# Kernel optimization log

Measured on AMD Instinct MI355X. Metric: run time of the kernel, lower is better.

The kernel has to match this reference:

```python
import jax, jax.numpy as jnp
import numpy as np
from jax import lax

B, C, H, W = 4, 256, 64, 64
R = 4  # reduction
BN_EPS = 1e-5


def setup_inputs() -> dict:
    key = jax.random.key(0)
    ks = jax.random.split(key, 18)
    n = jax.random.normal
    return {
        "x_self": n(ks[0], (B, C, H, W), jnp.float32),
        "x_other": n(ks[1], (B, C, H, W), jnp.float32),
        "q_w": n(ks[2], (C, C), jnp.float32) * 0.05,      # self_q 1x1 conv
        "q_b": n(ks[3], (C,), jnp.float32) * 0.05,
        "kv_w": n(ks[4], (2 * C, C), jnp.float32) * 0.05,  # other_kv 1x1 conv
        "kv_b": n(ks[5], (2 * C,), jnp.float32) * 0.05,
        "g1_w": n(ks[6], (C // R, C), jnp.float32) * 0.05,  # gate conv1
        "g1_b": n(ks[7], (C // R,), jnp.float32) * 0.05,
        "g2_w": n(ks[8], (1, C // R), jnp.float32) * 0.05,  # gate conv2
        "g2_b": n(ks[9], (1,), jnp.float32) * 0.05,
        "dw_w": n(ks[10], (C, 1, 3, 3), jnp.float32) * 0.1,  # depthwise 3x3
        "dw_b": n(ks[11], (C,), jnp.float32) * 0.05,
        "bn_g": jnp.ones((C,), jnp.float32),
        "bn_b": jnp.zeros((C,), jnp.float32),
        "bn_m": n(ks[12], (C,), jnp.float32) * 0.05,
        "bn_v": jax.random.uniform(ks[13], (C,), jnp.float32, 0.5, 1.5),
        "out_w": n(ks[14], (C, C), jnp.float32) * 0.05,
        "out_b": n(ks[15], (C,), jnp.float32) * 0.05,
    }


def _conv1x1(x, w, b):
    return jnp.einsum('bchw,oc->bohw', x, w) + b[None, :, None, None]


def reference(x_self, x_other, q_w, q_b, kv_w, kv_b, g1_w, g1_b, g2_w, g2_b,
              dw_w, dw_b, bn_g, bn_b, bn_m, bn_v, out_w, out_b):
    # local branch: depthwise 3x3 conv -> BatchNorm (eval stats) -> SiLU
    y = lax.conv_general_dilated(
        x_self, dw_w, (1, 1), 'SAME',
        feature_group_count=C,
        dimension_numbers=('NCHW', 'OIHW', 'NCHW')) + dw_b[None, :, None, None]
    scale = (bn_g / jnp.sqrt(bn_v + BN_EPS))[None, :, None, None]
    y = (y - bn_m[None, :, None, None]) * scale + bn_b[None, :, None, None]
    local_feat = y * jax.nn.sigmoid(y)  # SiLU

    # cross attention over HW tokens
    q = _conv1x1(x_self, q_w, q_b).reshape(B, C, H * W)
    kv = _conv1x1(x_other, kv_w, kv_b)
    k = kv[:, :C].reshape(B, C, H * W)
    v = kv[:, C:].reshape(B, C, H * W)
    attn = jnp.einsum('bcn,bcm->bnm', q, k) / jnp.sqrt(jnp.float32(C))  # [B,HW,HW]
    attn = jax.nn.softmax(attn, axis=-1)
    attn_out = jnp.einsum('bnm,bcm->bcn', attn, v).reshape(B, C, H, W)

    # channel-squeeze gate on x_self -> scalar per sample
    p = jnp.mean(x_self, axis=(2, 3))                 # [B,C] global avg pool
    g = jax.nn.relu(p @ g1_w.T + g1_b)                # [B,C//R]
    g = jax.nn.sigmoid(g @ g2_w.T + g2_b)             # [B,1]
    gate = g[:, :, None, None]

    fused = local_feat + gate * attn_out
    return _conv1x1(fused, out_w, out_b)
```

## Files before the change

### kernel.cpp

```cpp
#include <hip/hip_runtime.h>
#include <stdint.h>

#define BB 4
#define CC 256
#define HH 64
#define WWD 64
#define NN 4096
#define LOG2E 1.4426950408889634f

typedef __attribute__((ext_vector_type(8))) short short8;
typedef __attribute__((ext_vector_type(4))) float f32x4;
typedef __attribute__((ext_vector_type(16))) float f32x16;
typedef __attribute__((ext_vector_type(4))) unsigned short us4;
typedef unsigned long long ull;

__device__ __forceinline__ unsigned short f2bf(float f) {
  unsigned int u = __float_as_uint(f);
  u += 0x7fffu + ((u >> 16) & 1u);
  return (unsigned short)(u >> 16);
}
__device__ __forceinline__ float bf2f(unsigned short h) {
  return __uint_as_float(((unsigned int)h) << 16);
}
__device__ __forceinline__ short8 ld8(const unsigned short* p) {
  return *reinterpret_cast<const short8*>(p);
}
__device__ __forceinline__ unsigned char f2fp8(float v) {
  return (unsigned char)__builtin_amdgcn_cvt_pk_fp8_f32(v, v, 0, false);
}
__device__ __forceinline__ int rowmap(int reg, int h) {
  return (reg & 3) + 8 * (reg >> 2) + 4 * h;
}

__global__ __launch_bounds__(256, 2) void k_pre(
    const float* __restrict__ xs, const float* __restrict__ xo,
    const float* __restrict__ dww, const float* __restrict__ dwb,
    const float* __restrict__ bng, const float* __restrict__ bnb,
    const float* __restrict__ bnm, const float* __restrict__ bnv,
    const float* __restrict__ qw, const float* __restrict__ kvw,
    const float* __restrict__ ow, unsigned short* __restrict__ XtS,
    unsigned short* __restrict__ XtO, unsigned short* __restrict__ localT,
    float* __restrict__ psumA, unsigned short* __restrict__ Wb) {
  __shared__ float rb3[3][64][67];
  __shared__ unsigned short sb[64][67];
  int tid = threadIdx.x;
  if (blockIdx.z == 8) {
    int i = (blockIdx.x * 64 + blockIdx.y) * 1024 + tid * 4;
    const float* src;
    if (i < 65536) src = qw + i;
    else if (i < 196608) src = kvw + (i - 65536);
    else src = ow + (i - 196608);
    f32x4 v = *reinterpret_cast<const f32x4*>(src);
    us4 r;
#pragma unroll
    for (int j = 0; j < 4; ++j) r[j] = f2bf(v[j]);
    *reinterpret_cast<us4*>(Wb + i) = r;
    return;
  }
  int c0 = blockIdx.x * 64, h = blockIdx.y;
  int b = blockIdx.z >> 1, which = blockIdx.z & 1;
  const float* src = which ? xo : xs;
  int wq = tid >> 6, w = tid & 63;
  int dlo = which ? 1 : 0, dhi = which ? 1 : 2;
  for (int d = dlo; d <= dhi; ++d) {
    int hh = h + d - 1;
    bool ok = (hh >= 0 && hh < HH);
#pragma unroll
    for (int p = 0; p < 4; ++p) {
      int idx = p * 256 + tid;
      int cl = idx >> 4, ws4 = (idx & 15) * 4;
      f32x4 v = {};
      if (ok)
        v = *reinterpret_cast<const f32x4*>(
            &src[(((size_t)(b * CC + c0 + cl)) * HH + hh) * WWD + ws4]);
#pragma unroll
      for (int j = 0; j < 4; ++j) rb3[d][cl][ws4 + 1 + j] = v[j];
    }
    if (tid < 64) { rb3[d][tid][0] = 0.f; rb3[d][tid][65] = 0.f; }
  }
  __syncthreads();
  unsigned short* dst = which ? XtO : XtS;
  int n0 = h * 64, cb = (tid & 15) * 4;
#pragma unroll
  for (int i = 0; i < 4; ++i) {
    int wl = i * 16 + (tid >> 4);
    us4 r;
#pragma unroll
    for (int j = 0; j < 4; ++j) r[j] = f2bf(rb3[1][cb + j][wl + 1]);
    *reinterpret_cast<us4*>(&dst[((size_t)b * NN + n0 + wl) * CC + c0 + cb]) = r;
  }
  if (which) return;
  if (tid < 64) {
    float s = 0.f;
    for (int ww = 0; ww < 64; ++ww) s += rb3[1][tid][ww + 1];
    psumA[((size_t)(b * 64 + h)) * CC + c0 + tid] = s;
  }
  for (int p = 0; p < 16; ++p) {
    int cl = p * 4 + wq, c = c0 + cl;
    float acc = 0.f;
#pragma unroll
    for (int di = 0; di < 3; ++di)
#pragma unroll
      for (int dj = 0; dj < 3; ++dj)
        acc = fmaf(rb3[di][cl][w + dj], dww[c * 9 + di * 3 + dj], acc);
    float y = acc + dwb[c];
    float sc = bng[c] * rsqrtf(bnv[c] + 1e-5f);
    float v = (y - bnm[c]) * sc + bnb[c];
    sb[cl][w] = f2bf(v / (1.f + __expf(-v)));
  }
  __syncthreads();
#pragma unroll
  for (int i = 0; i < 4; ++i) {
    int wl = i * 16 + (tid >> 4);
    us4 r;
#pragma unroll
    for (int j = 0; j < 4; ++j) r[j] = sb[cb + j][wl];
    *reinterpret_cast<us4*>(&localT[((size_t)b * NN + h * WWD + wl) * CC + c0 + cb]) = r;
  }
}

__global__ __launch_bounds__(256, 4) void k_qkv(
    const unsigned short* __restrict__ XtS, const unsigned short* __restrict__ XtO,
    const unsigned short* __restrict__ Wb, const float* __restrict__ qb,
    const float* __restrict__ kvb, const float* __restrict__ psumA,
    const float* __restrict__ g1w, const float* __restrict__ g1b,
    const float* __restrict__ g2w, const float* __restrict__ g2b,
    unsigned char* __restrict__ Qt8, unsigned char* __restrict__ Kt8,
    unsigned char* __restrict__ Vv8, float* __restrict__ gate) {
  __shared__ unsigned short Xs[64][264];
  int tid = threadIdx.x;
  int id = blockIdx.y;
  if (id == 3) {
    if (blockIdx.x != 0 || blockIdx.z != 0) return;
    float* mf = (float*)&Xs[0][0];
    float* hpf = mf + 1024;
    int c = tid;
    for (int b4 = 0; b4 < 4; ++b4) {
      float s = 0.f;
      for (int hh = 0; hh < 64; ++hh) s += psumA[((size_t)(b4 * 64 + hh)) * CC + c];
      mf[b4 * 256 + c] = s * (1.f / 4096.f);
    }
    __syncthreads();
    for (int b4 = 0; b4 < 4; ++b4) {
      int j = tid >> 2, cq = tid & 3;
      float s = 0.f;
      for (int cc = cq * 64; cc < cq * 64 + 64; ++cc)
        s = fmaf(mf[b4 * 256 + cc], g1w[j * CC + cc], s);
      hpf[j * 5 + cq] = s;
      __syncthreads();
      if (tid < 64) {
        float hh = fmaxf(hpf[tid * 5] + hpf[tid * 5 + 1] + hpf[tid * 5 + 2] +
                             hpf[tid * 5 + 3] + g1b[tid], 0.f);
        float t = hh * g2w[tid];
        for (int off = 32; off; off >>= 1) t += __shfl_down(t, off, 64);
        if (tid == 0) gate[b4] = 1.f / (1.f + expf(-(t + g2b[0])));
      }
      __syncthreads();
    }
    return;
  }
  int n0 = blockIdx.x * 64, b = blockIdx.z;
  const unsigned short* Xt = (id == 0) ? XtS : XtO;
  const unsigned short* W = Wb + id * 65536;
  int wave = tid >> 6, lane = tid & 63, l31 = lane & 31, h = lane >> 5;
#pragma unroll
  for (int p = 0; p < 8; ++p) {
    int r = p * 8 + (tid >> 5), c = (tid & 31) * 8;
    *reinterpret_cast<uint4*>(&Xs[r][c]) =
        *reinterpret_cast<const uint4*>(Xt + ((size_t)b * NN + n0 + r) * CC + c);
  }
  __syncthreads();
  int o0 = wave * 64;
  f32x16 acc[4] = {};
  if (id < 2) {
#pragma unroll
    for (int t = 0; t < 16; ++t) {
      short8 a0 = ld8(&Xs[l31][t * 16 + h * 8]);
      short8 a1 = ld8(&Xs[32 + l31][t * 16 + h * 8]);
      short8 b0 = ld8(W + (size_t)(o0 + l31) * CC + t * 16 + h * 8);
      short8 b1 = ld8(W + (size_t)(o0 + 32 + l31) * CC + t * 16 + h * 8);
      acc[0] = __builtin_amdgcn_mfma_f32_32x32x16_bf16(a0, b0, acc[0], 0, 0, 0);
      acc[1] = __builtin_amdgcn_mfma_f32_32x32x16_bf16(a0, b1, acc[1], 0, 0, 0);
      acc[2] = __builtin_amdgcn_mfma_f32_32x32x16_bf16(a1, b0, acc[2], 0, 0, 0);
      acc[3] = __builtin_amdgcn_mfma_f32_32x32x16_bf16(a1, b1, acc[3], 0, 0, 0);
    }
    const float* bias = id ? kvb : qb;
    unsigned char* Out8 = id ? Kt8 : Qt8;
    __syncthreads();
    unsigned char (*T8)[264] = reinterpret_cast<unsigned char(*)[264]>(&Xs[0][0]);
#pragma unroll
    for (int nt = 0; nt < 2; ++nt)
#pragma unroll
      for (int ot = 0; ot < 2; ++ot) {
        int o = o0 + ot * 32 + l31;
        float bv = bias[o];
#pragma unroll
        for (int reg = 0; reg < 16; ++reg) {
          int nl = nt * 32 + rowmap(reg, h);
          T8[nl][o] = f2fp8((acc[nt * 2 + ot][reg] + bv) * 0.25f);
        }
      }
    __syncthreads();
#pragma unroll
    for (int p = 0; p < 4; ++p) {
      int idx = p * 256 + tid, row = idx >> 4, cc = (idx & 15) * 16;
      ull a0 = *reinterpret_cast<const ull*>(&T8[row][cc]);
      ull a1 = *reinterpret_cast<const ull*>(&T8[row][cc + 8]);
      uint4 u;
      u.x = (unsigned)a0; u.y = (unsigned)(a0 >> 32);
      u.z = (unsigned)a1; u.w = (unsigned)(a1 >> 32);
      *reinterpret_cast<uint4*>(Out8 + ((size_t)b * NN + n0 + row) * CC + cc) = u;
    }
  } else {
#pragma unroll
    for (int t = 0; t < 16; ++t) {
      short8 a0 = ld8(W + (size_t)(o0 + l31) * CC + t * 16 + h * 8);
      short8 a1 = ld8(W + (size_t)(o0 + 32 + l31) * CC + t * 16 + h * 8);
      short8 b0 = ld8(&Xs[l31][t * 16 + h * 8]);
      short8 b1 = ld8(&Xs[32 + l31][t * 16 + h * 8]);
      acc[0] = __builtin_amdgcn_mfma_f32_32x32x16_bf16(a0, b0, acc[0], 0, 0, 0);
      acc[1] = __builtin_amdgcn_mfma_f32_32x32x16_bf16(a0, b1, acc[1], 0, 0, 0);
      acc[2] = __builtin_amdgcn_mfma_f32_32x32x16_bf16(a1, b0, acc[2], 0, 0, 0);
      acc[3] = __builtin_amdgcn_mfma_f32_32x32x16_bf16(a1, b1, acc[3], 0, 0, 0);
    }
    __syncthreads();
    unsigned char (*V8)[72] = reinterpret_cast<unsigned char(*)[72]>(&Xs[0][0]);
#pragma unroll
    for (int ot = 0; ot < 2; ++ot)
#pragma unroll
      for (int nt = 0; nt < 2; ++nt)
#pragma unroll
        for (int reg = 0; reg < 16; ++reg) {
          int o = o0 + ot * 32 + rowmap(reg, h);
          int nl = nt * 32 + l31;
          V8[o][nl] = f2fp8(acc[ot * 2 + nt][reg] + kvb[CC + o]);
        }
    __syncthreads();
#pragma unroll
    for (int p = 0; p < 4; ++p) {
      int idx = p * 256 + tid, o = idx >> 2, mm = (idx & 3) * 16;
      ull a0 = *reinterpret_cast<const ull*>(&V8[o][mm]);
      ull a1 = *reinterpret_cast<const ull*>(&V8[o][mm + 8]);
      uint4 u;
      u.x = (unsigned)a0; u.y = (unsigned)(a0 >> 32);
      u.z = (unsigned)a1; u.w = (unsigned)(a1 >> 32);
      *reinterpret_cast<uint4*>(Vv8 + ((size_t)b * CC + o) * NN + n0 + mm) = u;
    }
  }
}

__global__ __launch_bounds__(256, 3) void k_flash8(
    const unsigned char* __restrict__ Qt8, const unsigned char* __restrict__ Kt8,
    const unsigned char* __restrict__ Vv8, const unsigned short* __restrict__ localT,
    const float* __restrict__ gate, unsigned short* __restrict__ Opart16,
    float* __restrict__ Lpart, unsigned short* __restrict__ fusedT) {
  __shared__ unsigned char Ks8[64][264];
  __shared__ unsigned char Vs8[256][72];
  __shared__ unsigned char Ps8[64][72];
  __shared__ float lred[2][64];
  __shared__ float ltot[64];
  int b = blockIdx.x & 3, n0 = (blockIdx.x >> 2) * 64;
  int sp = blockIdx.y, nsp = gridDim.y;
  int tid = threadIdx.x, wave = tid >> 6, lane = tid & 63, l31 = lane & 31, h = lane >> 5;
  int rw = wave & 1, cw = wave >> 1;
  const unsigned char* qp = Qt8 + ((size_t)b * NN + n0 + rw * 32 + l31) * CC + h * 8;
  long qf[16];
#pragma unroll
  for (int t = 0; t < 16; ++t) qf[t] = *reinterpret_cast<const long*>(qp + t * 16);
  f32x16 O[4] = {};
  float lacc[16] = {};
  int m_lo = (64 * sp) / nsp, m_hi = (64 * (sp + 1)) / nsp;
  for (int mt = m_lo; mt < m_hi; ++mt) {
    int m0 = mt * 64;
    __syncthreads();
#pragma unroll
    for (int p = 0; p < 4; ++p) {
      int idx = p * 256 + tid, m = idx >> 4, cc = (idx & 15) * 16;
      const ull* gp = reinterpret_cast<const ull*>(Kt8 + ((size_t)b * NN + m0 + m) * CC + cc);
      ull a0 = gp[0], a1 = gp[1];
      *reinterpret_cast<ull*>(&Ks8[m][cc]) = a0;
      *reinterpret_cast<ull*>(&Ks8[m][cc + 8]) = a1;
    }
#pragma unroll
    for (int p = 0; p < 4; ++p) {
      int idx = p * 256 + tid, c = idx >> 2, mm = (idx & 3) * 16;
      const ull* gp = reinterpret_cast<const ull*>(Vv8 + ((size_t)b * CC + c) * NN + m0 + mm);
      ull a0 = gp[0], a1 = gp[1];
      *reinterpret_cast<ull*>(&Vs8[c][mm]) = a0;
      *reinterpret_cast<ull*>(&Vs8[c][mm + 8]) = a1;
    }
    __syncthreads();
    f32x16 S = {};
#pragma unroll
    for (int t = 0; t < 16; ++t) {
      long kf = *reinterpret_cast<const long*>(&Ks8[cw * 32 + l31][t * 16 + h * 8]);
      S = __builtin_amdgcn_mfma_f32_32x32x16_fp8_fp8(qf[t], kf, S, 0, 0, 0);
    }
#pragma unroll
    for (int reg = 0; reg < 16; ++reg) {
      float p = __builtin_exp2f(S[reg] * LOG2E);
      lacc[reg] += p;
      Ps8[rw * 32 + rowmap(reg, h)][cw * 32 + l31] = f2fp8(p);
    }
    __syncthreads();
#pragma unroll
    for (int t = 0; t < 4; ++t) {
      long pf = *reinterpret_cast<const long*>(&Ps8[rw * 32 + l31][t * 16 + h * 8]);
#pragma unroll
      for (int ct = 0; ct < 4; ++ct) {
        long vf = *reinterpret_cast<const long*>(&Vs8[cw * 128 + ct * 32 + l31][t * 16 + h * 8]);
        O[ct] = __builtin_amdgcn_mfma_f32_32x32x16_fp8_fp8(pf, vf, O[ct], 0, 0, 0);
      }
    }
  }
#pragma unroll
  for (int reg = 0; reg < 16; ++reg) {
    float v = lacc[reg];
#pragma unroll
    for (int msk = 1; msk < 32; msk <<= 1) v += __shfl_xor(v, msk, 64);
    lacc[reg] = v;
  }
  __syncthreads();
#pragma unroll
  for (int g = 0; g < 16; ++g)
    if (l31 == g) lred[cw][rw * 32 + rowmap(g, h)] = lacc[g];
  __syncthreads();
  size_t obase2 = (size_t)(b * nsp + sp) * NN;
  if (nsp == 1) {
    if (tid < 64) ltot[tid] = lred[0][tid] + lred[1][tid];
    __syncthreads();
    float gv = gate[b];
    float inv[16];
#pragma unroll
    for (int reg = 0; reg < 16; ++reg)
      inv[reg] = gv / ltot[rw * 32 + rowmap(reg, h)];
#pragma unroll
    for (int ct = 0; ct < 4; ++ct)
#pragma unroll
      for (int reg = 0; reg < 16; ++reg) {
        int n = n0 + rw * 32 + rowmap(reg, h);
        int c = cw * 128 + ct * 32 + l31;
        size_t idx = ((size_t)b * NN + n) * CC + c;
        fusedT[idx] = f2bf(bf2f(localT[idx]) + O[ct][reg] * inv[reg]);
      }
  } else {
    if (tid < 64) Lpart[obase2 + n0 + tid] = lred[0][tid] + lred[1][tid];
#pragma unroll
    for (int ct = 0; ct < 4; ++ct)
#pragma unroll
      for (int reg = 0; reg < 16; ++reg) {
        int n = n0 + rw * 32 + rowmap(reg, h);
        int c = cw * 128 + ct * 32 + l31;
        Opart16[(obase2 + n) * CC + c] = f2bf(O[ct][reg]);
      }
  }
}

__global__ __launch_bounds__(256, 4) void k_out(
    const unsigned short* __restrict__ W, const float* __restrict__ ob,
    const float* __restrict__ gate, const unsigned short* __restrict__ localT,
    const unsigned short* __restrict__ Opart16, const float* __restrict__ Lpart,
    const unsigned short* __restrict__ fusedT, float* __restrict__ out, int nsp) {
  __shared__ unsigned short Xs[64][264];
  int n0 = blockIdx.x * 64, o0 = blockIdx.y * 128, b = blockIdx.z;
  int tid = threadIdx.x, wave = tid >> 6, lane = tid & 63, l31 = lane & 31, h = lane >> 5;
  if (Opart16) {
    float gv = gate[b];
#pragma unroll
    for (int p = 0; p < 8; ++p) {
      int r = p * 8 + (tid >> 5), cc = (tid & 31) * 8;
      int n = n0 + r;
      float lsum = 0.f;
      for (int sp = 0; sp < nsp; ++sp) lsum += Lpart[(size_t)(b * nsp + sp) * NN + n];
      float g = gv / lsum;
      float ov[8] = {};
      for (int sp = 0; sp < nsp; ++sp) {
        short8 x = ld8(Opart16 + ((size_t)(b * nsp + sp) * NN + n) * CC + cc);
#pragma unroll
        for (int j = 0; j < 8; ++j) ov[j] += bf2f(((unsigned short*)&x)[j]);
      }
      const unsigned short* lp = localT + ((size_t)b * NN + n) * CC + cc;
      short8 lv = ld8(lp);
      us4 r0, r1;
#pragma unroll
      for (int j = 0; j < 4; ++j) {
        r0[j] = f2bf(bf2f(((unsigned short*)&lv)[j]) + ov[j] * g);
        r1[j] = f2bf(bf2f(((unsigned short*)&lv)[j + 4]) + ov[j + 4] * g);
      }
      *reinterpret_cast<us4*>(&Xs[r][cc]) = r0;
      *reinterpret_cast<us4*>(&Xs[r][cc + 4]) = r1;
    }
  } else {
#pragma unroll
    for (int p = 0; p < 8; ++p) {
      int r = p * 8 + (tid >> 5), c = (tid & 31) * 8;
      *reinterpret_cast<uint4*>(&Xs[r][c]) =
          *reinterpret_cast<const uint4*>(fusedT + ((size_t)b * NN + n0 + r) * CC + c);
    }
  }
  int obase = o0 + wave * 32;
  short8 af[16];
#pragma unroll
  for (int t = 0; t < 16; ++t) af[t] = ld8(W + (size_t)(obase + l31) * CC + t * 16 + h * 8);
  __syncthreads();
  f32x16 acc[2] = {};
#pragma unroll
  for (int t = 0; t < 16; ++t) {
    short8 b0 = ld8(&Xs[l31][t * 16 + h * 8]);
    short8 b1 = ld8(&Xs[32 + l31][t * 16 + h * 8]);
    acc[0] = __builtin_amdgcn_mfma_f32_32x32x16_bf16(af[t], b0, acc[0], 0, 0, 0);
    acc[1] = __builtin_amdgcn_mfma_f32_32x32x16_bf16(af[t], b1, acc[1], 0, 0, 0);
  }
#pragma unroll
  for (int nt = 0; nt < 2; ++nt)
#pragma unroll
    for (int reg = 0; reg < 16; ++reg) {
      int o = obase + rowmap(reg, h);
      int n = n0 + nt * 32 + l31;
      out[((size_t)b * CC + o) * NN + n] = acc[nt][reg] + ob[o];
    }
}

extern "C" void kernel_launch(void* const* d_in, const int* in_sizes, int n_in,
                              void* d_out, int out_size, void* d_ws, size_t ws_size,
                              hipStream_t stream) {
  const float* xs  = (const float*)d_in[0];
  const float* xo  = (const float*)d_in[1];
  const float* qw  = (const float*)d_in[2];
  const float* qb  = (const float*)d_in[3];
  const float* kvw = (const float*)d_in[4];
  const float* kvb = (const float*)d_in[5];
  const float* g1w = (const float*)d_in[6];
  const float* g1b = (const float*)d_in[7];
  const float* g2w = (const float*)d_in[8];
  const float* g2b = (const float*)d_in[9];
  const float* dww = (const float*)d_in[10];
  const float* dwb = (const float*)d_in[11];
  const float* bng = (const float*)d_in[12];
  const float* bnb = (const float*)d_in[13];
  const float* bnm = (const float*)d_in[14];
  const float* bnv = (const float*)d_in[15];
  const float* ow  = (const float*)d_in[16];
  const float* ob  = (const float*)d_in[17];
  float* out = (float*)d_out;
  char* ws = (char*)d_ws;

  const size_t SZ  = (size_t)BB * NN * CC * 2;
  const size_t SZ8 = (size_t)BB * NN * CC;
  unsigned short* XtS    = (unsigned short*)(ws);
  unsigned short* XtO    = (unsigned short*)(ws + SZ);
  unsigned short* localT = (unsigned short*)(ws + 2 * SZ);
  unsigned char*  Qt8    = (unsigned char*)(ws + 3 * SZ);
  unsigned char*  Kt8    = (unsigned char*)(ws + 3 * SZ + SZ8);
  unsigned char*  Vv8    = (unsigned char*)(ws + 3 * SZ + 2 * SZ8);
  unsigned short* Wb     = (unsigned short*)(ws + 3 * SZ + 3 * SZ8);
  float* psumA = (float*)(ws + 3 * SZ + 3 * SZ8 + 524288);
  float* gate  = (float*)(ws + 3 * SZ + 3 * SZ8 + 524288 + 262144);
  size_t tail  = 3 * SZ + 3 * SZ8 + 524288 + 262144 + 4096;
  float* Lpart = (float*)(ws + tail);
  unsigned short* Opart16 = (unsigned short*)(ws + tail + 262144);
  unsigned short* fusedT = XtS;

  size_t base = tail + 262144;
  int S = 1;
  if (ws_size >= base + 3ull * SZ) S = 3;
  else if (ws_size >= base + 2ull * SZ) S = 2;

  k_pre<<<dim3(4, 64, 9), 256, 0, stream>>>(xs, xo, dww, dwb, bng, bnb, bnm, bnv,
                                            qw, kvw, ow, XtS, XtO, localT, psumA, Wb);
  k_qkv<<<dim3(64, 4, 4), 256, 0, stream>>>(XtS, XtO, Wb, qb, kvb, psumA,
                                            g1w, g1b, g2w, g2b, Qt8, Kt8, Vv8, gate);
  k_flash8<<<dim3(256, S), 256, 0, stream>>>(Qt8, Kt8, Vv8, localT, gate, Opart16,
                                             Lpart, fusedT);
  k_out<<<dim3(64, 2, 4), 256, 0, stream>>>(Wb + 196608, ob, gate, localT,
                                            S > 1 ? Opart16 : nullptr, Lpart, fusedT,
                                            out, S);
}
```

Baseline: 251.6 us.

## Store Q/K in MFMA fragment layout and read them directly from global in flash kernel

Result: slower. 325.9 us (+29.5%).

```diff
diff --git a/kernel.cpp b/kernel.cpp
--- a/kernel.cpp
+++ b/kernel.cpp
@@ -202,14 +202,15 @@
       }
     __syncthreads();
 #pragma unroll
-    for (int p = 0; p < 4; ++p) {
-      int idx = p * 256 + tid, row = idx >> 4, cc = (idx & 15) * 16;
-      ull a0 = *reinterpret_cast<const ull*>(&T8[row][cc]);
-      ull a1 = *reinterpret_cast<const ull*>(&T8[row][cc + 8]);
-      uint4 u;
-      u.x = (unsigned)a0; u.y = (unsigned)(a0 >> 32);
-      u.z = (unsigned)a1; u.w = (unsigned)(a1 >> 32);
-      *reinterpret_cast<uint4*>(Out8 + ((size_t)b * NN + n0 + row) * CC + cc) = u;
+    for (int p = 0; p < 8; ++p) {
+      int idx = p * 256 + tid;
+      int msel = idx >> 10, rem = idx & 1023;
+      int kt = rem >> 6, li = rem & 63;
+      int row = (li & 31) + 32 * msel;
+      int col = kt * 16 + (li >> 5) * 8;
+      ull v = *reinterpret_cast<const ull*>(&T8[row][col]);
+      *reinterpret_cast<ull*>(
+          Out8 + (((size_t)b * 128 + (n0 >> 5) + msel) * 16 + kt) * 512 + li * 8) = v;
     }
   } else {
 #pragma unroll
@@ -249,12 +250,11 @@
   }
 }
 
-__global__ __launch_bounds__(256, 3) void k_flash8(
+__global__ __launch_bounds__(256, 4) void k_flash8(
     const unsigned char* __restrict__ Qt8, const unsigned char* __restrict__ Kt8,
     const unsigned char* __restrict__ Vv8, const unsigned short* __restrict__ localT,
     const float* __restrict__ gate, unsigned short* __restrict__ Opart16,
     float* __restrict__ Lpart, unsigned short* __restrict__ fusedT) {
-  __shared__ unsigned char Ks8[64][264];
   __shared__ unsigned char Vs8[256][72];
   __shared__ unsigned char Ps8[64][72];
   __shared__ float lred[2][64];
@@ -263,38 +263,36 @@
   int sp = blockIdx.y, nsp = gridDim.y;
   int tid = threadIdx.x, wave = tid >> 6, lane = tid & 63, l31 = lane & 31, h = lane >> 5;
   int rw = wave & 1, cw = wave >> 1;
-  const unsigned char* qp = Qt8 + ((size_t)b * NN + n0 + rw * 32 + l31) * CC + h * 8;
-  long qf[16];
-#pragma unroll
-  for (int t = 0; t < 16; ++t) qf[t] = *reinterpret_cast<const long*>(qp + t * 16);
+  const unsigned char* qbase =
+      Qt8 + (((size_t)b * 128 + (n0 >> 5) + rw) * 16) * 512 + lane * 8;
   f32x16 O[4] = {};
   float lacc[16] = {};
   int m_lo = (64 * sp) / nsp, m_hi = (64 * (sp + 1)) / nsp;
   for (int mt = m_lo; mt < m_hi; ++mt) {
     int m0 = mt * 64;
     __syncthreads();
-#pragma unroll
-    for (int p = 0; p < 4; ++p) {
-      int idx = p * 256 + tid, m = idx >> 4, cc = (idx & 15) * 16;
-      const ull* gp = reinterpret_cast<const ull*>(Kt8 + ((size_t)b * NN + m0 + m) * CC + cc);
-      ull a0 = gp[0], a1 = gp[1];
-      *reinterpret_cast<ull*>(&Ks8[m][cc]) = a0;
-      *reinterpret_cast<ull*>(&Ks8[m][cc + 8]) = a1;
-    }
+    uint4 vreg[4];
 #pragma unroll
     for (int p = 0; p < 4; ++p) {
       int idx = p * 256 + tid, c = idx >> 2, mm = (idx & 3) * 16;
-      const ull* gp = reinterpret_cast<const ull*>(Vv8 + ((size_t)b * CC + c) * NN + m0 + mm);
-      ull a0 = gp[0], a1 = gp[1];
-      *reinterpret_cast<ull*>(&Vs8[c][mm]) = a0;
-      *reinterpret_cast<ull*>(&Vs8[c][mm + 8]) = a1;
-    }
-    __syncthreads();
+      vreg[p] = *reinterpret_cast<const uint4*>(Vv8 + ((size_t)b * CC + c) * NN + m0 + mm);
+    }
+    const unsigned char* kb =
+        Kt8 + (((size_t)b * 128 + (mt * 2 + cw)) * 16) * 512 + lane * 8;
     f32x16 S = {};
 #pragma unroll
     for (int t = 0; t < 16; ++t) {
-      long kf = *reinterpret_cast<const long*>(&Ks8[cw * 32 + l31][t * 16 + h * 8]);
-      S = __builtin_amdgcn_mfma_f32_32x32x16_fp8_fp8(qf[t], kf, S, 0, 0, 0);
+      long qf = *reinterpret_cast<const long*>(qbase + t * 512);
+      long kf = *reinterpret_cast<const long*>(kb + t * 512);
+      S = __builtin_amdgcn_mfma_f32_32x32x16_fp8_fp8(qf, kf, S, 0, 0, 0);
+    }
+#pragma unroll
+    for (int p = 0; p < 4; ++p) {
+      int idx = p * 256 + tid, c = idx >> 2, mm = (idx & 3) * 16;
+      ull lo = ((ull)vreg[p].y << 32) | vreg[p].x;
+      ull hi = ((ull)vreg[p].w << 32) | vreg[p].z;
+      *reinterpret_cast<ull*>(&Vs8[c][mm]) = lo;
+      *reinterpret_cast<ull*>(&Vs8[c][mm + 8]) = hi;
     }
 #pragma unroll
     for (int reg = 0; reg < 16; ++reg) {
@@ -463,7 +461,8 @@
 
   size_t base = tail + 262144;
   int S = 1;
-  if (ws_size >= base + 3ull * SZ) S = 3;
+  if (ws_size >= base + 4ull * SZ) S = 4;
+  else if (ws_size >= base + 3ull * SZ) S = 3;
   else if (ws_size >= base + 2ull * SZ) S = 2;
 
   k_pre<<<dim3(4, 64, 9), 256, 0, stream>>>(xs, xo, dww, dwb, bng, bnb, bnm, bnv,
```

## Process four rows per k_pre block with bf16 shared halo buffer

Applied to the files above, without the earlier changes.

Result: slower. 271.7 us (+8.0%).

```diff
diff --git a/kernel.cpp b/kernel.cpp
--- a/kernel.cpp
+++ b/kernel.cpp
@@ -41,81 +41,97 @@
     const float* __restrict__ ow, unsigned short* __restrict__ XtS,
     unsigned short* __restrict__ XtO, unsigned short* __restrict__ localT,
     float* __restrict__ psumA, unsigned short* __restrict__ Wb) {
-  __shared__ float rb3[3][64][67];
-  __shared__ unsigned short sb[64][67];
+  __shared__ unsigned short rb[6][64][68];
+  __shared__ unsigned short sb[64][68];
   int tid = threadIdx.x;
   if (blockIdx.z == 8) {
-    int i = (blockIdx.x * 64 + blockIdx.y) * 1024 + tid * 4;
-    const float* src;
-    if (i < 65536) src = qw + i;
-    else if (i < 196608) src = kvw + (i - 65536);
-    else src = ow + (i - 196608);
-    f32x4 v = *reinterpret_cast<const f32x4*>(src);
-    us4 r;
-#pragma unroll
-    for (int j = 0; j < 4; ++j) r[j] = f2bf(v[j]);
-    *reinterpret_cast<us4*>(Wb + i) = r;
+    int base = (blockIdx.x * 16 + blockIdx.y) * 4096 + tid * 4;
+#pragma unroll
+    for (int q = 0; q < 4; ++q) {
+      int i = base + q * 1024;
+      const float* src;
+      if (i < 65536) src = qw + i;
+      else if (i < 196608) src = kvw + (i - 65536);
+      else src = ow + (i - 196608);
+      f32x4 v = *reinterpret_cast<const f32x4*>(src);
+      us4 r;
+#pragma unroll
+      for (int j = 0; j < 4; ++j) r[j] = f2bf(v[j]);
+      *reinterpret_cast<us4*>(Wb + i) = r;
+    }
     return;
   }
-  int c0 = blockIdx.x * 64, h = blockIdx.y;
+  int c0 = blockIdx.x * 64, h0 = blockIdx.y * 4;
   int b = blockIdx.z >> 1, which = blockIdx.z & 1;
   const float* src = which ? xo : xs;
-  int wq = tid >> 6, w = tid & 63;
-  int dlo = which ? 1 : 0, dhi = which ? 1 : 2;
-  for (int d = dlo; d <= dhi; ++d) {
-    int hh = h + d - 1;
+  int rlo = which ? 1 : 0, rhi = which ? 4 : 5;
+  for (int r = rlo; r <= rhi; ++r) {
+    int hh = h0 + r - 1;
     bool ok = (hh >= 0 && hh < HH);
 #pragma unroll
     for (int p = 0; p < 4; ++p) {
       int idx = p * 256 + tid;
-      int cl = idx >> 4, ws4 = (idx & 15) * 4;
+      int cl = idx >> 4, w4 = (idx & 15) * 4;
       f32x4 v = {};
       if (ok)
         v = *reinterpret_cast<const f32x4*>(
-            &src[(((size_t)(b * CC + c0 + cl)) * HH + hh) * WWD + ws4]);
-#pragma unroll
-      for (int j = 0; j < 4; ++j) rb3[d][cl][ws4 + 1 + j] = v[j];
-    }
-    if (tid < 64) { rb3[d][tid][0] = 0.f; rb3[d][tid][65] = 0.f; }
+            &src[(((size_t)(b * CC + c0 + cl)) * HH + hh) * WWD + w4]);
+      us4 rr;
+#pragma unroll
+      for (int j = 0; j < 4; ++j) rr[j] = f2bf(v[j]);
+      *reinterpret_cast<us4*>(&rb[r][cl][w4]) = rr;
+    }
   }
   __syncthreads();
   unsigned short* dst = which ? XtO : XtS;
-  int n0 = h * 64, cb = (tid & 15) * 4;
-#pragma unroll
+  int cb = (tid & 15) * 4;
   for (int i = 0; i < 4; ++i) {
-    int wl = i * 16 + (tid >> 4);
-    us4 r;
-#pragma unroll
-    for (int j = 0; j < 4; ++j) r[j] = f2bf(rb3[1][cb + j][wl + 1]);
-    *reinterpret_cast<us4*>(&dst[((size_t)b * NN + n0 + wl) * CC + c0 + cb]) = r;
+    int n0 = (h0 + i) * 64;
+#pragma unroll
+    for (int i2 = 0; i2 < 4; ++i2) {
+      int wl = i2 * 16 + (tid >> 4);
+      us4 r;
+#pragma unroll
+      for (int j = 0; j < 4; ++j) r[j] = rb[1 + i][cb + j][wl];
+      *reinterpret_cast<us4*>(&dst[((size_t)b * NN + n0 + wl) * CC + c0 + cb]) = r;
+    }
   }
   if (which) return;
-  if (tid < 64) {
+  {
+    int c = tid & 63, i = tid >> 6;
     float s = 0.f;
-    for (int ww = 0; ww < 64; ++ww) s += rb3[1][tid][ww + 1];
-    psumA[((size_t)(b * 64 + h)) * CC + c0 + tid] = s;
-  }
-  for (int p = 0; p < 16; ++p) {
-    int cl = p * 4 + wq, c = c0 + cl;
-    float acc = 0.f;
-#pragma unroll
-    for (int di = 0; di < 3; ++di)
-#pragma unroll
-      for (int dj = 0; dj < 3; ++dj)
-        acc = fmaf(rb3[di][cl][w + dj], dww[c * 9 + di * 3 + dj], acc);
-    float y = acc + dwb[c];
-    float sc = bng[c] * rsqrtf(bnv[c] + 1e-5f);
-    float v = (y - bnm[c]) * sc + bnb[c];
-    sb[cl][w] = f2bf(v / (1.f + __expf(-v)));
-  }
-  __syncthreads();
-#pragma unroll
+    for (int w = 0; w < 64; ++w) s += bf2f(rb[1 + i][c][w]);
+    psumA[((size_t)(b * 64 + h0 + i)) * CC + c0 + c] = s;
+  }
+  int wq = tid >> 6, w = tid & 63;
   for (int i = 0; i < 4; ++i) {
-    int wl = i * 16 + (tid >> 4);
-    us4 r;
-#pragma unroll
-    for (int j = 0; j < 4; ++j) r[j] = sb[cb + j][wl];
-    *reinterpret_cast<us4*>(&localT[((size_t)b * NN + h * WWD + wl) * CC + c0 + cb]) = r;
+    for (int p = 0; p < 16; ++p) {
+      int cl = p * 4 + wq, c = c0 + cl;
+      float acc = 0.f;
+#pragma unroll
+      for (int di = 0; di < 3; ++di)
+#pragma unroll
+        for (int dj = 0; dj < 3; ++dj) {
+          int ww = w + dj - 1;
+          float xv = (ww >= 0 && ww < 64) ? bf2f(rb[i + di][cl][ww]) : 0.f;
+          acc = fmaf(xv, dww[c * 9 + di * 3 + dj], acc);
+        }
+      float y = acc + dwb[c];
+      float sc = bng[c] * rsqrtf(bnv[c] + 1e-5f);
+      float v = (y - bnm[c]) * sc + bnb[c];
+      sb[cl][w] = f2bf(v / (1.f + __expf(-v)));
+    }
+    __syncthreads();
+#pragma unroll
+    for (int i2 = 0; i2 < 4; ++i2) {
+      int wl = i2 * 16 + (tid >> 4);
+      us4 r;
+#pragma unroll
+      for (int j = 0; j < 4; ++j) r[j] = sb[cb + j][wl];
+      *reinterpret_cast<us4*>(
+          &localT[((size_t)b * NN + (h0 + i) * 64 + wl) * CC + c0 + cb]) = r;
+    }
+    __syncthreads();
   }
 }
 
@@ -466,7 +482,7 @@
   if (ws_size >= base + 3ull * SZ) S = 3;
   else if (ws_size >= base + 2ull * SZ) S = 2;
 
-  k_pre<<<dim3(4, 64, 9), 256, 0, stream>>>(xs, xo, dww, dwb, bng, bnb, bnm, bnv,
+  k_pre<<<dim3(4, 16, 9), 256, 0, stream>>>(xs, xo, dww, dwb, bng, bnb, bnm, bnv,
                                             qw, kvw, ow, XtS, XtO, localT, psumA, Wb);
   k_qkv<<<dim3(64, 4, 4), 256, 0, stream>>>(XtS, XtO, Wb, qb, kvb, psumA,
                                             g1w, g1b, g2w, g2b, Qt8, Kt8, Vv8, gate);
```
